# Kernel tuning notes

Hardware: AMD Instinct MI355X
Metric: run time of the kernel (lower is better)

Reference implementation:

```python
import jax, jax.numpy as jnp
import numpy as np

N = 8192  # number of DAG nodes


def setup_inputs() -> dict:
    key = jax.random.key(0)
    k1, k2, k3 = jax.random.split(key, 3)
    thresholds = jax.random.normal(k1, (N,), dtype=jnp.float32)
    # children in [-1, N): -1 marks a leaf (no child)
    left = jax.random.randint(k2, (N,), -1, N, dtype=jnp.int32)
    right = jax.random.randint(k3, (N,), -1, N, dtype=jnp.int32)
    return {"thresholds": thresholds, "left": left, "right": right}


def reference(thresholds, left, right):
    # BFS fixed-point reachability from node 0, N sequential relaxation steps.
    n_nodes = left.shape[0]

    def step(reachable, _):
        # route children of reachable non-leaf nodes into a scatter; dump
        # inactive slots into the sentinel index n_nodes (dropped on slice)
        active_left = jnp.where(reachable & (left >= 0), left, n_nodes)
        active_right = jnp.where(reachable & (right >= 0), right, n_nodes)
        new_reachable = jnp.zeros(n_nodes + 1, dtype=jnp.bool_)
        new_reachable = new_reachable.at[active_left].set(True)
        new_reachable = new_reachable.at[active_right].set(True)
        new_reachable = new_reachable.at[0].set(True)
        return (new_reachable[:n_nodes] | reachable, None)

    init = jnp.zeros(n_nodes, dtype=jnp.bool_).at[0].set(True)
    mask, _ = jax.lax.scan(step, init, None, length=n_nodes)
    return mask
```

## Files before the change

### kernel.cpp

```cpp
#include <hip/hip_runtime.h>


#define NMAX 8192
#define BLK  1024

__global__ __launch_bounds__(BLK) void dag_reach_kernel(
    const int* __restrict__ left,
    const int* __restrict__ right,
    int* __restrict__ out,
    int n)
{
    __shared__ int sL[NMAX];
    __shared__ int sR[NMAX];
    __shared__ unsigned int reach[NMAX / 32];
    __shared__ int s_changed;

    const int tid = threadIdx.x;

    for (int i = tid; i < n; i += BLK) {
        sL[i] = left[i];
        sR[i] = right[i];
    }
    for (int i = tid; i < NMAX / 32; i += BLK) reach[i] = 0u;
    __syncthreads();
    if (tid == 0) reach[0] = 1u;

    unsigned int myExp = 0u;
    const int base = tid * 8;
    __syncthreads();

    while (true) {
        if (tid == 0) s_changed = 0;
        __syncthreads();

        unsigned int word = reach[tid >> 2];
        unsigned int pend = ((word >> ((tid & 3) * 8)) & 0xFFu) & ~myExp;

        if (pend && base < n) {
            s_changed = 1;
            myExp |= pend;
            while (pend) {
                int b = __ffs(pend) - 1;
                pend &= pend - 1;
                int node = base + b;
                if (node < n) {
                    int l = sL[node];
                    int r = sR[node];
                    if (l >= 0) atomicOr(&reach[l >> 5], 1u << (l & 31));
                    if (r >= 0) atomicOr(&reach[r >> 5], 1u << (r & 31));
                }
            }
        }
        __syncthreads();
        if (!s_changed) break;
    }

    for (int i = tid; i < n; i += BLK) {
        out[i] = (int)((reach[i >> 5] >> (i & 31)) & 1u);
    }
}

extern "C" void kernel_launch(void* const* d_in, const int* in_sizes, int n_in,
                              void* d_out, int out_size, void* d_ws, size_t ws_size,
                              hipStream_t stream)
{
    const int* left  = (const int*)d_in[1];
    const int* right = (const int*)d_in[2];
    int* out = (int*)d_out;
    const int n = in_sizes[1];

    dag_reach_kernel<<<1, BLK, 0, stream>>>(left, right, out, n);
}
```

Baseline: 72.22 us.

## Replace bitmask fixed-point sweep with frontier-queue BFS using wave-aggregated enqueue

Swaps the repeated full-bitmap scan for a level-synchronous BFS. An explicit shared-memory frontier queue is filled through atomicOr on the visited bitmap and a wave-ballot aggregated atomicAdd on the tail. Each level now handles only newly discovered nodes rather than rescanning every node, and left/right are packed into int2 with vectorized int4 loads and stores. Block size drops to 256 threads. The number of barrier rounds still depends on graph depth, and the int4 paths assume n is a multiple of 4.

```diff
diff --git a/kernel.cpp b/kernel.cpp
--- a/kernel.cpp
+++ b/kernel.cpp
@@ -2,7 +2,7 @@
 
 
 #define NMAX 8192
-#define BLK  1024
+#define BLK  256
 
 __global__ __launch_bounds__(BLK) void dag_reach_kernel(
     const int* __restrict__ left,
@@ -10,53 +10,93 @@
     int* __restrict__ out,
     int n)
 {
-    __shared__ int sL[NMAX];
-    __shared__ int sR[NMAX];
-    __shared__ unsigned int reach[NMAX / 32];
-    __shared__ int s_changed;
+    __shared__ int2 sLR[NMAX];
+    __shared__ int  Q[NMAX];
+    __shared__ unsigned int vis[NMAX / 32];
+    __shared__ int s_tail;
+    __shared__ int s_end;
 
-    const int tid = threadIdx.x;
+    const int tid  = threadIdx.x;
+    const int lane = tid & 63;
 
-    for (int i = tid; i < n; i += BLK) {
-        sL[i] = left[i];
-        sR[i] = right[i];
+    for (int i = 4 * tid; i < n; i += 4 * BLK) {
+        int4 l4 = *reinterpret_cast<const int4*>(left  + i);
+        int4 r4 = *reinterpret_cast<const int4*>(right + i);
+        sLR[i + 0] = make_int2(l4.x, r4.x);
+        sLR[i + 1] = make_int2(l4.y, r4.y);
+        sLR[i + 2] = make_int2(l4.z, r4.z);
+        sLR[i + 3] = make_int2(l4.w, r4.w);
     }
-    for (int i = tid; i < NMAX / 32; i += BLK) reach[i] = 0u;
-    __syncthreads();
-    if (tid == 0) reach[0] = 1u;
-
-    unsigned int myExp = 0u;
-    const int base = tid * 8;
+    for (int i = tid; i < NMAX / 32; i += BLK) vis[i] = 0u;
     __syncthreads();
 
+    if (tid == 0) {
+        vis[0] = 1u;
+        Q[0]   = 0;
+        s_tail = 1;
+    }
+
+    int head = 0;
     while (true) {
-        if (tid == 0) s_changed = 0;
+        if (tid == 0) s_end = s_tail;
         __syncthreads();
+        const int end = s_end;
+        if (head == end) break;
 
-        unsigned int word = reach[tid >> 2];
-        unsigned int pend = ((word >> ((tid & 3) * 8)) & 0xFFu) & ~myExp;
+        for (int i = head + tid; i < end; i += BLK) {
+            const int  v  = Q[i];
+            const int2 lr = sLR[v];
 
-        if (pend && base < n) {
-            s_changed = 1;
-            myExp |= pend;
-            while (pend) {
-                int b = __ffs(pend) - 1;
-                pend &= pend - 1;
-                int node = base + b;
-                if (node < n) {
-                    int l = sL[node];
-                    int r = sR[node];
-                    if (l >= 0) atomicOr(&reach[l >> 5], 1u << (l & 31));
-                    if (r >= 0) atomicOr(&reach[r >> 5], 1u << (r & 31));
+            const int cl = lr.x;
+            bool pushL = false;
+            if (cl >= 0) {
+                const unsigned bit = 1u << (cl & 31);
+                const unsigned old = atomicOr(&vis[cl >> 5], bit);
+                pushL = (old & bit) == 0u;
+            }
+            unsigned long long bL = __ballot(pushL);
+            if (bL) {
+                const int leader = __ffsll(bL) - 1;
+                int base = 0;
+                if (lane == leader) base = atomicAdd(&s_tail, __popcll(bL));
+                base = __shfl(base, leader);
+                if (pushL) {
+                    const int idx = base + __popcll(bL & ((1ull << lane) - 1ull));
+                    Q[idx] = cl;
+                }
+            }
+
+            const int cr = lr.y;
+            bool pushR = false;
+            if (cr >= 0) {
+                const unsigned bit = 1u << (cr & 31);
+                const unsigned old = atomicOr(&vis[cr >> 5], bit);
+                pushR = (old & bit) == 0u;
+            }
+            unsigned long long bR = __ballot(pushR);
+            if (bR) {
+                const int leader = __ffsll(bR) - 1;
+                int base = 0;
+                if (lane == leader) base = atomicAdd(&s_tail, __popcll(bR));
+                base = __shfl(base, leader);
+                if (pushR) {
+                    const int idx = base + __popcll(bR & ((1ull << lane) - 1ull));
+                    Q[idx] = cr;
                 }
             }
         }
+        head = end;
         __syncthreads();
-        if (!s_changed) break;
     }
 
-    for (int i = tid; i < n; i += BLK) {
-        out[i] = (int)((reach[i >> 5] >> (i & 31)) & 1u);
+    for (int i = 4 * tid; i < n; i += 4 * BLK) {
+        const unsigned w = vis[i >> 5];
+        const int b = i & 31;
+        *reinterpret_cast<int4*>(out + i) =
+            make_int4((int)((w >> (b + 0)) & 1u),
+                      (int)((w >> (b + 1)) & 1u),
+                      (int)((w >> (b + 2)) & 1u),
+                      (int)((w >> (b + 3)) & 1u));
     }
 }
 
```

After: 83.57 us. 15.7% more time.

## Restructure DAG reachability with 32-node ownership, inner sweeps, batched child fetches

Applied to the files above, without the earlier changes.

Shrinks the block to 256 threads, each owning one full 32-bit reach word, and runs several inner sweeps per barrier round by re-reading the volatile bitset, so newly reached nodes can be expanded without waiting for a block-wide sync. Left/right children are interleaved into an int2 shared array, loaded with int4 vector loads, and pending nodes are processed four at a time to overlap shared-memory reads. Output is written with vectorized int4 stores. The change trades per-thread parallelism (more serial work per thread) for fewer barriers, and assumes n is a multiple of 4 and that n ≤ 8192 with exactly 256 words.

```diff
diff --git a/kernel.cpp b/kernel.cpp
--- a/kernel.cpp
+++ b/kernel.cpp
@@ -1,8 +1,10 @@
 #include <hip/hip_runtime.h>
 
 
-#define NMAX 8192
-#define BLK  1024
+#define NMAX   8192
+#define BLK    256
+#define NWORDS (NMAX / 32)
+#define INNER  4
 
 __global__ __launch_bounds__(BLK) void dag_reach_kernel(
     const int* __restrict__ left,
@@ -10,53 +12,78 @@
     int* __restrict__ out,
     int n)
 {
-    __shared__ int sL[NMAX];
-    __shared__ int sR[NMAX];
-    __shared__ unsigned int reach[NMAX / 32];
+    __shared__ int2 sLR[NMAX];
+    __shared__ unsigned int reach[NWORDS];
     __shared__ int s_changed;
 
     const int tid = threadIdx.x;
 
-    for (int i = tid; i < n; i += BLK) {
-        sL[i] = left[i];
-        sR[i] = right[i];
+    for (int i = 4 * tid; i < n; i += 4 * BLK) {
+        int4 l4 = *reinterpret_cast<const int4*>(left  + i);
+        int4 r4 = *reinterpret_cast<const int4*>(right + i);
+        sLR[i + 0] = make_int2(l4.x, r4.x);
+        sLR[i + 1] = make_int2(l4.y, r4.y);
+        sLR[i + 2] = make_int2(l4.z, r4.z);
+        sLR[i + 3] = make_int2(l4.w, r4.w);
     }
-    for (int i = tid; i < NMAX / 32; i += BLK) reach[i] = 0u;
+    reach[tid] = (tid == 0) ? 1u : 0u;
     __syncthreads();
-    if (tid == 0) reach[0] = 1u;
 
-    unsigned int myExp = 0u;
-    const int base = tid * 8;
-    __syncthreads();
+    unsigned int expanded = 0u;
+    const int base = tid * 32;
+    volatile unsigned int* vreach = reach;
 
     while (true) {
         if (tid == 0) s_changed = 0;
         __syncthreads();
 
-        unsigned int word = reach[tid >> 2];
-        unsigned int pend = ((word >> ((tid & 3) * 8)) & 0xFFu) & ~myExp;
-
-        if (pend && base < n) {
-            s_changed = 1;
-            myExp |= pend;
-            while (pend) {
-                int b = __ffs(pend) - 1;
-                pend &= pend - 1;
-                int node = base + b;
-                if (node < n) {
-                    int l = sL[node];
-                    int r = sR[node];
-                    if (l >= 0) atomicOr(&reach[l >> 5], 1u << (l & 31));
-                    if (r >= 0) atomicOr(&reach[r >> 5], 1u << (r & 31));
+        int localChanged = 0;
+        #pragma unroll
+        for (int it = 0; it < INNER; ++it) {
+            unsigned int pend = vreach[tid] & ~expanded;
+            if (pend) {
+                localChanged = 1;
+                expanded |= pend;
+                while (pend) {
+                    int b0 = __ffs(pend) - 1; pend &= pend - 1;
+                    int b1 = -1, b2 = -1, b3 = -1;
+                    if (pend) { b1 = __ffs(pend) - 1; pend &= pend - 1;
+                        if (pend) { b2 = __ffs(pend) - 1; pend &= pend - 1;
+                            if (pend) { b3 = __ffs(pend) - 1; pend &= pend - 1; } } }
+                    int2 lr0 = sLR[base + b0];
+                    int2 lr1 = sLR[base + (b1 < 0 ? b0 : b1)];
+                    int2 lr2 = sLR[base + (b2 < 0 ? b0 : b2)];
+                    int2 lr3 = sLR[base + (b3 < 0 ? b0 : b3)];
+                    if (lr0.x >= 0) atomicOr(&reach[lr0.x >> 5], 1u << (lr0.x & 31));
+                    if (lr0.y >= 0) atomicOr(&reach[lr0.y >> 5], 1u << (lr0.y & 31));
+                    if (b1 >= 0) {
+                        if (lr1.x >= 0) atomicOr(&reach[lr1.x >> 5], 1u << (lr1.x & 31));
+                        if (lr1.y >= 0) atomicOr(&reach[lr1.y >> 5], 1u << (lr1.y & 31));
+                    }
+                    if (b2 >= 0) {
+                        if (lr2.x >= 0) atomicOr(&reach[lr2.x >> 5], 1u << (lr2.x & 31));
+                        if (lr2.y >= 0) atomicOr(&reach[lr2.y >> 5], 1u << (lr2.y & 31));
+                    }
+                    if (b3 >= 0) {
+                        if (lr3.x >= 0) atomicOr(&reach[lr3.x >> 5], 1u << (lr3.x & 31));
+                        if (lr3.y >= 0) atomicOr(&reach[lr3.y >> 5], 1u << (lr3.y & 31));
+                    }
                 }
             }
         }
+        if (localChanged) s_changed = 1;
         __syncthreads();
         if (!s_changed) break;
     }
 
-    for (int i = tid; i < n; i += BLK) {
-        out[i] = (int)((reach[i >> 5] >> (i & 31)) & 1u);
+    for (int i = 4 * tid; i < n; i += 4 * BLK) {
+        const unsigned w = reach[i >> 5];
+        const int b = i & 31;
+        *reinterpret_cast<int4*>(out + i) =
+            make_int4((int)((w >> (b + 0)) & 1u),
+                      (int)((w >> (b + 1)) & 1u),
+                      (int)((w >> (b + 2)) & 1u),
+                      (int)((w >> (b + 3)) & 1u));
     }
 }
 
```

Result: slower. 74.89 us (+3.7%).
